# Kernel optimization log

Measured on AMD Instinct MI355X. Metric: run time of the kernel, lower is better.

## Reference

```python
import jax, jax.numpy as jnp
import numpy as np
from jax.scipy.special import logsumexp

EPS = 0.1
MAX_ITER = 50
THRESH = 1e-9


def _cost_matrix(x, y, p=2):
    # |x_i - y_j|^p summed over feature dim -> (N, P1, P2)
    return jnp.sum(jnp.abs(x[:, :, None, :] - y[:, None, :, :]) ** p, axis=-1)


def _sinkhorn_uv(C, eps, max_iter):
    # Log-domain Sinkhorn iterations; C is treated as a constant (torch no_grad).
    N, P1, P2 = C.shape
    log_mu = jnp.log(jnp.full((N, P1), 1.0 / P1, C.dtype) + 1e-8)
    log_nu = jnp.log(jnp.full((N, P2), 1.0 / P2, C.dtype) + 1e-8)

    def M(u, v):
        return (-C + u[:, :, None] + v[:, None, :]) / eps

    def cond(state):
        u, v, err, it = state
        return jnp.logical_and(it < max_iter, err >= THRESH)

    def body(state):
        u, v, err, it = state
        u1 = u
        u = eps * (log_mu - logsumexp(M(u, v), axis=-1)) + u
        v = eps * (log_nu - logsumexp(M(u, v), axis=-2)) + v
        err = jnp.mean(jnp.sum(jnp.abs(u - u1), axis=-1))
        return (u, v, err, it + 1)

    u0 = jnp.zeros((N, P1), C.dtype)
    v0 = jnp.zeros((N, P2), C.dtype)
    u, v, _, _ = jax.lax.while_loop(cond, body, (u0, v0, jnp.inf, 0))
    return u, v


def setup_inputs() -> dict:
    key = jax.random.key(0)
    kx, ky = jax.random.split(key)
    x = jax.random.normal(kx, (4, 2048, 64), dtype=jnp.float32)
    y = jax.random.normal(ky, (4, 2048, 64), dtype=jnp.float32)
    return {"x": x, "y": y}


def reference(x, y):
    C = _cost_matrix(x, y)
    # u, v computed under no_grad in torch -> constants w.r.t. x, y
    U, V = _sinkhorn_uv(jax.lax.stop_gradient(C), EPS, MAX_ITER)
    pi = jnp.exp((-C + U[:, :, None] + V[:, None, :]) / EPS)
    cost = jnp.sum(pi * C, axis=(-2, -1))  # reduction='none' -> (N,)
    return (cost, pi, C)
```

## Files before the change

### kernel.cpp

```cpp
#include <hip/hip_runtime.h>
#include <math.h>

#define NB 4
#define P 2048
#define DF 64
#define EPS 0.1f
#define INV_EPS 10.0f
#define MAX_ITER 50
#define NBLK 256
#define TPB 512
#define TR 128
#define TC 256
#define SCALE 14.426950408889634f
#define C2N 0.069314718055994531f
#define RPF (NB * P * 8)
#define CPF (NB * P * 16)

typedef float vfloat4 __attribute__((ext_vector_type(4)));

#if __has_builtin(__builtin_amdgcn_exp2f)
#define EXP2(x) __builtin_amdgcn_exp2f(x)
#else
#define EXP2(x) exp2f(x)
#endif
#if __has_builtin(__builtin_amdgcn_logf)
#define LOG2(x) __builtin_amdgcn_logf(x)
#else
#define LOG2(x) log2f(x)
#endif

struct BuildMem { float xs[32 * 132]; float ys[32 * 260]; };
union IterBuf {
  float rin[8 * 132];
  float Ld[64 * 260];
  float cin[16 * 260];
};
struct SMem {
  union { BuildMem b; IterBuf ib; } u;
  float red[132];
  float vlds[2][260];
};

__device__ __forceinline__ void flag_store(unsigned* f, unsigned v) {
  __hip_atomic_store(f, v, __ATOMIC_RELAXED, __HIP_MEMORY_SCOPE_AGENT);
}
__device__ __forceinline__ unsigned flag_load(unsigned* f) {
  return __hip_atomic_load(f, __ATOMIC_RELAXED, __HIP_MEMORY_SCOPE_AGENT);
}
__device__ __forceinline__ void store_f2_agent(float* p, float a, float b) {
  unsigned long long bits =
      ((unsigned long long)__float_as_uint(b) << 32) | __float_as_uint(a);
  __hip_atomic_store((unsigned long long*)p, bits, __ATOMIC_RELAXED,
                     __HIP_MEMORY_SCOPE_AGENT);
}
__device__ __forceinline__ float2 load_f2_agent(const float* p) {
  unsigned long long bits = __hip_atomic_load((unsigned long long*)p,
      __ATOMIC_RELAXED, __HIP_MEMORY_SCOPE_AGENT);
  return make_float2(__uint_as_float((unsigned)bits),
                     __uint_as_float((unsigned)(bits >> 32)));
}
__device__ __forceinline__ void store_f_agent(float* p, float v) {
  __hip_atomic_store(p, v, __ATOMIC_RELAXED, __HIP_MEMORY_SCOPE_AGENT);
}

__device__ __forceinline__ void u_stage(
    int k, int t, int c8, int r0, int ti, int tj, int n,
    const float (&cr)[2][32], const float* vl,
    float* rpp, unsigned* rf_mine) {
  float vv[32];
#pragma unroll
  for (int i = 0; i < 32; ++i) vv[i] = vl[32 * (i >> 2) + 4 * c8 + (i & 3)];
  float Lr[2];
#pragma unroll
  for (int r = 0; r < 2; ++r) {
    float m = -3.4e38f;
#pragma unroll
    for (int i = 0; i < 32; ++i) m = fmaxf(m, vv[i] - cr[r][i]);
    m = fmaxf(m, __shfl_xor(m, 1));
    m = fmaxf(m, __shfl_xor(m, 2));
    m = fmaxf(m, __shfl_xor(m, 4));
    float s = 0.f;
#pragma unroll
    for (int i = 0; i < 32; ++i) s += EXP2(vv[i] - cr[r][i] - m);
    s += __shfl_xor(s, 1);
    s += __shfl_xor(s, 2);
    s += __shfl_xor(s, 4);
    Lr[r] = m + LOG2(s);
  }
  if (c8 == 0)
    store_f2_agent(rpp + ((n * 16 + ti) * 8 + tj) * TR + r0, Lr[0], Lr[1]);
  __threadfence_block();
  __syncthreads();
  if (t == 0) flag_store(rf_mine, (unsigned)(k + 1));
}

__device__ __forceinline__ void row_merge(
    int k, int t, int r0, int ti, int n,
    float (&Ucr)[2], const float* rpp, unsigned* rfb, SMem& sm, float l2mu) {
  if (t < 8) {
    while (flag_load(rfb + t) < (unsigned)(k + 1)) __builtin_amdgcn_s_sleep(1);
  }
  __syncthreads();
  {
    const int idx = 2 * t;
    float2 a = load_f2_agent(rpp + (n * 16 + ti) * 1024 + idx);
    const int j = idx >> 7, row = idx & 127;
    *(float2*)&sm.u.ib.rin[j * 132 + row] = a;
  }
  __syncthreads();
  if (t < 128) {
    float m = sm.u.ib.rin[t];
#pragma unroll
    for (int j = 1; j < 8; ++j) m = fmaxf(m, sm.u.ib.rin[j * 132 + t]);
    float s = 0.f;
#pragma unroll
    for (int j = 0; j < 8; ++j) s += EXP2(sm.u.ib.rin[j * 132 + t] - m);
    sm.red[t] = l2mu - (m + LOG2(s));
  }
  __syncthreads();
  Ucr[0] = sm.red[r0];
  Ucr[1] = sm.red[r0 + 1];
}

__device__ __forceinline__ void v_stage(
    int k, int t, int w, int gg, int c8, int ti, int tj, int n,
    const float (&cr)[2][32], const float (&Ucr)[2],
    float* cpp, unsigned* cf_mine, SMem& sm) {
  const int grp = 8 * w + gg;
#pragma unroll
  for (int i = 0; i < 32; ++i) {
    float a0 = Ucr[0] - cr[0][i];
    float a1 = Ucr[1] - cr[1][i];
    float pm = fmaxf(a0, a1);
    float ps = 1.f + EXP2(-fabsf(a0 - a1));
    sm.u.ib.Ld[grp * 260 + 32 * (i >> 2) + 4 * c8 + (i & 3)] = pm + LOG2(ps);
  }
  __syncthreads();
  if (t < TC) {
    float m = sm.u.ib.Ld[t];
#pragma unroll
    for (int g2 = 1; g2 < 64; ++g2) m = fmaxf(m, sm.u.ib.Ld[g2 * 260 + t]);
    float s = 0.f;
#pragma unroll
    for (int g2 = 0; g2 < 64; ++g2) s += EXP2(sm.u.ib.Ld[g2 * 260 + t] - m);
    store_f_agent(cpp + ((n * 8 + tj) * 16 + ti) * TC + t, m + LOG2(s));
  }
  __threadfence_block();
  __syncthreads();
  if (t == 0) flag_store(cf_mine, (unsigned)(k + 1));
}

__device__ __forceinline__ void col_merge(
    int k, int t, int tj, int n, float* vl,
    const float* cpp, unsigned* cfb, SMem& sm, float l2mu) {
  if (t < 16) {
    while (flag_load(cfb + t) < (unsigned)(k + 1)) __builtin_amdgcn_s_sleep(1);
  }
  __syncthreads();
  {
    const int idx = 8 * t;
    const int jj = idx >> 8, col = idx & 255;
    const float* src = cpp + (n * 8 + tj) * 4096 + idx;
    float2 a = load_f2_agent(src);
    float2 b2 = load_f2_agent(src + 2);
    float2 c2 = load_f2_agent(src + 4);
    float2 d2 = load_f2_agent(src + 6);
    vfloat4 v0 = {a.x, a.y, b2.x, b2.y};
    vfloat4 v1 = {c2.x, c2.y, d2.x, d2.y};
    *(vfloat4*)&sm.u.ib.cin[jj * 260 + col] = v0;
    *(vfloat4*)&sm.u.ib.cin[jj * 260 + col + 4] = v1;
  }
  __syncthreads();
  if (t < TC) {
    float m = sm.u.ib.cin[t];
#pragma unroll
    for (int j = 1; j < 16; ++j) m = fmaxf(m, sm.u.ib.cin[j * 260 + t]);
    float s = 0.f;
#pragma unroll
    for (int j = 0; j < 16; ++j) s += EXP2(sm.u.ib.cin[j * 260 + t] - m);
    vl[t] = l2mu - (m + LOG2(s));
  }
  __syncthreads();
}

__global__ __launch_bounds__(TPB, 2) void sinkhorn_all(
    const float* __restrict__ x, const float* __restrict__ y,
    float* __restrict__ Cout, float* __restrict__ pi,
    float* __restrict__ cost, float* __restrict__ rp,
    float* __restrict__ cp, unsigned* __restrict__ flags, float l2mu) {
  __shared__ SMem sm;
  const int t = threadIdx.x;
  const int w = t >> 6;
  const int l = t & 63;
  const int gg = l >> 3;
  const int c8 = l & 7;
  const int b = blockIdx.x;
  const int g = b >> 7;
  const int idx = b & 127;
  const int ti = idx >> 3;
  const int tj = idx & 7;
  const int nA = 2 * g, nB = 2 * g + 1;
  const int r0 = 16 * w + 2 * gg;
  unsigned* rfA_mine = flags + (nA * 16 + ti) * 8 + tj;
  unsigned* rfB_mine = flags + (nB * 16 + ti) * 8 + tj;
  unsigned* rfA_band = flags + (nA * 16 + ti) * 8;
  unsigned* rfB_band = flags + (nB * 16 + ti) * 8;
  unsigned* cfA_mine = flags + 512 + (nA * 8 + tj) * 16 + ti;
  unsigned* cfB_mine = flags + 512 + (nB * 8 + tj) * 16 + ti;
  unsigned* cfA_band = flags + 512 + (nA * 8 + tj) * 16;
  unsigned* cfB_band = flags + 512 + (nB * 8 + tj) * 16;
  unsigned* ef = flags + 1024;

  float creg[2][2][32];
  float U[2][2];

#pragma unroll
  for (int c = 0; c < 2; ++c) {
    const int n = 2 * g + c;
    const size_t xyb = (size_t)n * P * DF;
#pragma unroll
    for (int r = 0; r < 2; ++r)
#pragma unroll
      for (int i = 0; i < 32; ++i) creg[c][r][i] = 0.f;
#pragma unroll
    for (int h = 0; h < 2; ++h) {
      __syncthreads();
      {
        const int cl = t >> 2, db = (t & 3) * 8;
        const float* xp = x + xyb + (size_t)(TR * ti + cl) * DF + 32 * h + db;
        float4 q0 = *(const float4*)(xp);
        float4 q1 = *(const float4*)(xp + 4);
        float* xs = sm.u.b.xs;
        xs[(db + 0) * 132 + cl] = q0.x; xs[(db + 1) * 132 + cl] = q0.y;
        xs[(db + 2) * 132 + cl] = q0.z; xs[(db + 3) * 132 + cl] = q0.w;
        xs[(db + 4) * 132 + cl] = q1.x; xs[(db + 5) * 132 + cl] = q1.y;
        xs[(db + 6) * 132 + cl] = q1.z; xs[(db + 7) * 132 + cl] = q1.w;
      }
      {
        const int cl = t >> 1, db = (t & 1) * 16;
        const float* yp = y + xyb + (size_t)(TC * tj + cl) * DF + 32 * h + db;
        float4 q0 = *(const float4*)(yp + 0);
        float4 q1 = *(const float4*)(yp + 4);
        float4 q2 = *(const float4*)(yp + 8);
        float4 q3 = *(const float4*)(yp + 12);
        float* ys = sm.u.b.ys;
        ys[(db + 0) * 260 + cl] = q0.x;  ys[(db + 1) * 260 + cl] = q0.y;
        ys[(db + 2) * 260 + cl] = q0.z;  ys[(db + 3) * 260 + cl] = q0.w;
        ys[(db + 4) * 260 + cl] = q1.x;  ys[(db + 5) * 260 + cl] = q1.y;
        ys[(db + 6) * 260 + cl] = q1.z;  ys[(db + 7) * 260 + cl] = q1.w;
        ys[(db + 8) * 260 + cl] = q2.x;  ys[(db + 9) * 260 + cl] = q2.y;
        ys[(db + 10) * 260 + cl] = q2.z; ys[(db + 11) * 260 + cl] = q2.w;
        ys[(db + 12) * 260 + cl] = q3.x; ys[(db + 13) * 260 + cl] = q3.y;
        ys[(db + 14) * 260 + cl] = q3.z; ys[(db + 15) * 260 + cl] = q3.w;
      }
      __syncthreads();
#pragma unroll 4
      for (int dd = 0; dd < 32; ++dd) {
        float2 x2 = *(const float2*)&sm.u.b.xs[dd * 132 + r0];
#pragma unroll
        for (int cc = 0; cc < 8; ++cc) {
          float4 y4 = *(const float4*)&sm.u.b.ys[dd * 260 + 32 * cc + 4 * c8];
          float d0, d1;
          d0 = x2.x - y4.x; creg[c][0][4*cc+0] = fmaf(d0, d0, creg[c][0][4*cc+0]);
          d1 = x2.y - y4.x; creg[c][1][4*cc+0] = fmaf(d1, d1, creg[c][1][4*cc+0]);
          d0 = x2.x - y4.y; creg[c][0][4*cc+1] = fmaf(d0, d0, creg[c][0][4*cc+1]);
          d1 = x2.y - y4.y; creg[c][1][4*cc+1] = fmaf(d1, d1, creg[c][1][4*cc+1]);
          d0 = x2.x - y4.z; creg[c][0][4*cc+2] = fmaf(d0, d0, creg[c][0][4*cc+2]);
          d1 = x2.y - y4.z; creg[c][1][4*cc+2] = fmaf(d1, d1, creg[c][1][4*cc+2]);
          d0 = x2.x - y4.w; creg[c][0][4*cc+3] = fmaf(d0, d0, creg[c][0][4*cc+3]);
          d1 = x2.y - y4.w; creg[c][1][4*cc+3] = fmaf(d1, d1, creg[c][1][4*cc+3]);
        }
      }
    }
    const size_t cb = (size_t)n * P * P;
#pragma unroll
    for (int r = 0; r < 2; ++r) {
      const size_t rowb = cb + (size_t)(TR * ti + r0 + r) * P + TC * tj;
#pragma unroll
      for (int cc = 0; cc < 8; ++cc) {
        vfloat4 c4 = {creg[c][r][4*cc+0], creg[c][r][4*cc+1],
                      creg[c][r][4*cc+2], creg[c][r][4*cc+3]};
        __builtin_nontemporal_store(c4, (vfloat4*)(Cout + rowb + 32*cc + 4*c8));
        creg[c][r][4*cc+0] *= SCALE;
        creg[c][r][4*cc+1] *= SCALE;
        creg[c][r][4*cc+2] *= SCALE;
        creg[c][r][4*cc+3] *= SCALE;
      }
    }
  }
  __syncthreads();
  if (t < 256) { sm.vlds[0][t] = 0.f; sm.vlds[1][t] = 0.f; }
  __syncthreads();

  float* vlA = sm.vlds[0];
  float* vlB = sm.vlds[1];
  u_stage(0, t, c8, r0, ti, tj, nA, creg[0], vlA, rp + RPF, rfA_mine);
  u_stage(0, t, c8, r0, ti, tj, nB, creg[1], vlB, rp + RPF, rfB_mine);
#pragma unroll 1
  for (int k = 0; k < MAX_ITER; ++k) {
    const int pw = (k + 1) & 1;
    float* rpp = rp + pw * RPF;
    float* cpp = cp + pw * CPF;
    float* rpn = rp + (k & 1) * RPF;
    row_merge(k, t, r0, ti, nA, U[0], rpp, rfA_band, sm, l2mu);
    v_stage(k, t, w, gg, c8, ti, tj, nA, creg[0], U[0], cpp, cfA_mine, sm);
    row_merge(k, t, r0, ti, nB, U[1], rpp, rfB_band, sm, l2mu);
    v_stage(k, t, w, gg, c8, ti, tj, nB, creg[1], U[1], cpp, cfB_mine, sm);
    col_merge(k, t, tj, nA, vlA, cpp, cfA_band, sm, l2mu);
    if (k + 1 < MAX_ITER)
      u_stage(k + 1, t, c8, r0, ti, tj, nA, creg[0], vlA, rpn, rfA_mine);
    col_merge(k, t, tj, nB, vlB, cpp, cfB_band, sm, l2mu);
    if (k + 1 < MAX_ITER)
      u_stage(k + 1, t, c8, r0, ti, tj, nB, creg[1], vlB, rpn, rfB_mine);
  }

  if (t == 0) flag_store(&ef[b], 1u);
  if (t < 256) {
    while (flag_load(&ef[t]) < 1u) __builtin_amdgcn_s_sleep(1);
  }
  __syncthreads();
#pragma unroll
  for (int c = 0; c < 2; ++c) {
    const int n = 2 * g + c;
    float vv[32];
#pragma unroll
    for (int i = 0; i < 32; ++i)
      vv[i] = sm.vlds[c][32 * (i >> 2) + 4 * c8 + (i & 3)];
    float csum = 0.f;
#pragma unroll
    for (int r = 0; r < 2; ++r) {
      const size_t rowb = (size_t)n * P * P + (size_t)(TR*ti + r0 + r) * P + TC*tj;
#pragma unroll
      for (int cc = 0; cc < 8; ++cc) {
        vfloat4 p4;
        p4.x = EXP2(U[c][r] + vv[4*cc+0] - creg[c][r][4*cc+0]);
        p4.y = EXP2(U[c][r] + vv[4*cc+1] - creg[c][r][4*cc+1]);
        p4.z = EXP2(U[c][r] + vv[4*cc+2] - creg[c][r][4*cc+2]);
        p4.w = EXP2(U[c][r] + vv[4*cc+3] - creg[c][r][4*cc+3]);
        csum += p4.x * creg[c][r][4*cc+0] + p4.y * creg[c][r][4*cc+1]
              + p4.z * creg[c][r][4*cc+2] + p4.w * creg[c][r][4*cc+3];
        __builtin_nontemporal_store(p4, (vfloat4*)(pi + rowb + 32*cc + 4*c8));
      }
    }
    float cs = csum * C2N;
#pragma unroll
    for (int off = 32; off; off >>= 1) cs += __shfl_xor(cs, off);
    if (l == 0) atomicAdd(cost + n, cs);
  }
}

__global__ __launch_bounds__(256) void build_c(const float* __restrict__ x,
                                               const float* __restrict__ y,
                                               float* __restrict__ C,
                                               float* __restrict__ CT) {
  __shared__ float xs[DF][68];
  __shared__ float ys[DF][68];
  const int n = blockIdx.z;
  const int i0 = blockIdx.y * 64, j0 = blockIdx.x * 64;
  const int t = threadIdx.x;
  const int lr = t >> 4, c4 = (t & 15) * 4;
  const size_t xb = (size_t)n * P * DF;
  for (int rr = lr; rr < 64; rr += 16) {
    float4 xv = *(const float4*)(x + xb + (size_t)(i0 + rr) * DF + c4);
    float4 yv = *(const float4*)(y + xb + (size_t)(j0 + rr) * DF + c4);
    xs[c4 + 0][rr] = xv.x; xs[c4 + 1][rr] = xv.y;
    xs[c4 + 2][rr] = xv.z; xs[c4 + 3][rr] = xv.w;
    ys[c4 + 0][rr] = yv.x; ys[c4 + 1][rr] = yv.y;
    ys[c4 + 2][rr] = yv.z; ys[c4 + 3][rr] = yv.w;
  }
  __syncthreads();
  const int ty = t >> 4, tx = t & 15;
  float acc[4][4];
#pragma unroll
  for (int e = 0; e < 4; ++e)
#pragma unroll
    for (int f = 0; f < 4; ++f) acc[e][f] = 0.f;
#pragma unroll 4
  for (int d = 0; d < DF; ++d) {
    float4 a4 = *(const float4*)&xs[d][4 * ty];
    float4 b4 = *(const float4*)&ys[d][4 * tx];
    float av[4] = {a4.x, a4.y, a4.z, a4.w};
    float bv[4] = {b4.x, b4.y, b4.z, b4.w};
#pragma unroll
    for (int e = 0; e < 4; ++e)
#pragma unroll
      for (int f = 0; f < 4; ++f) {
        float df = av[e] - bv[f];
        acc[e][f] = fmaf(df, df, acc[e][f]);
      }
  }
  const size_t cbase = (size_t)n * P * P;
#pragma unroll
  for (int e = 0; e < 4; ++e) {
    float4 v4 = make_float4(acc[e][0], acc[e][1], acc[e][2], acc[e][3]);
    *(float4*)(C + cbase + (size_t)(i0 + 4 * ty + e) * P + (j0 + 4 * tx)) = v4;
  }
#pragma unroll
  for (int f = 0; f < 4; ++f) {
    float4 v4 = make_float4(acc[0][f], acc[1][f], acc[2][f], acc[3][f]);
    *(float4*)(CT + cbase + (size_t)(j0 + 4 * tx + f) * P + (i0 + 4 * ty)) = v4;
  }
}

__global__ __launch_bounds__(256) void lse_pass(const float* __restrict__ M,
                                                const float* __restrict__ wv_,
                                                float* __restrict__ out,
                                                float log_w) {
  __shared__ float red[8];
  const int b = blockIdx.x;
  const int n = b >> 11;
  const int t = threadIdx.x;
  const float4* row = (const float4*)(M + (size_t)b * P);
  const float4* wv = (const float4*)(wv_ + (size_t)n * P);
  float4 c0 = row[t], c1 = row[t + 256];
  float4 w0 = wv[t], w1 = wv[t + 256];
  float a[8];
  a[0] = (w0.x - c0.x) * INV_EPS; a[1] = (w0.y - c0.y) * INV_EPS;
  a[2] = (w0.z - c0.z) * INV_EPS; a[3] = (w0.w - c0.w) * INV_EPS;
  a[4] = (w1.x - c1.x) * INV_EPS; a[5] = (w1.y - c1.y) * INV_EPS;
  a[6] = (w1.z - c1.z) * INV_EPS; a[7] = (w1.w - c1.w) * INV_EPS;
  float mx = a[0];
#pragma unroll
  for (int k = 1; k < 8; ++k) mx = fmaxf(mx, a[k]);
#pragma unroll
  for (int o = 32; o > 0; o >>= 1) mx = fmaxf(mx, __shfl_xor(mx, o));
  if ((t & 63) == 0) red[t >> 6] = mx;
  __syncthreads();
  mx = fmaxf(fmaxf(red[0], red[1]), fmaxf(red[2], red[3]));
  float s = 0.f;
#pragma unroll
  for (int k = 0; k < 8; ++k) s += __expf(a[k] - mx);
#pragma unroll
  for (int o = 32; o > 0; o >>= 1) s += __shfl_xor(s, o);
  if ((t & 63) == 0) red[4 + (t >> 6)] = s;
  __syncthreads();
  if (t == 0) {
    float S = red[4] + red[5] + red[6] + red[7];
    out[b] = EPS * (log_w - (mx + __logf(S)));
  }
}

__global__ __launch_bounds__(256) void final_pass(const float* __restrict__ C,
                                                  const float* __restrict__ u,
                                                  const float* __restrict__ v,
                                                  float* __restrict__ pi,
                                                  float* __restrict__ cost) {
  __shared__ float red[4];
  const int b = blockIdx.x;
  const int n = b >> 11;
  const int t = threadIdx.x;
  const float ui = u[b];
  const float4* row = (const float4*)(C + (size_t)b * P);
  const float4* vv = (const float4*)(v + (size_t)n * P);
  float4* prow = (float4*)(pi + (size_t)b * P);
  float local = 0.f;
#pragma unroll
  for (int h = 0; h < 2; ++h) {
    float4 c = row[t + 256 * h];
    float4 vw = vv[t + 256 * h];
    float4 p;
    p.x = __expf((ui + vw.x - c.x) * INV_EPS);
    p.y = __expf((ui + vw.y - c.y) * INV_EPS);
    p.z = __expf((ui + vw.z - c.z) * INV_EPS);
    p.w = __expf((ui + vw.w - c.w) * INV_EPS);
    prow[t + 256 * h] = p;
    local += p.x * c.x + p.y * c.y + p.z * c.z + p.w * c.w;
  }
#pragma unroll
  for (int o = 32; o > 0; o >>= 1) local += __shfl_xor(local, o);
  if ((t & 63) == 0) red[t >> 6] = local;
  __syncthreads();
  if (t == 0) {
    float S = red[0] + red[1] + red[2] + red[3];
    atomicAdd(cost + n, S);
  }
}

extern "C" void kernel_launch(void* const* d_in, const int* in_sizes, int n_in,
                              void* d_out, int out_size, void* d_ws, size_t ws_size,
                              hipStream_t stream) {
  const float* x = (const float*)d_in[0];
  const float* y = (const float*)d_in[1];
  float* cost = (float*)d_out;
  float* pi = cost + 4;
  float* C = pi + (size_t)NB * P * P;
  float* rp = pi;
  float* cp = pi + 2 * RPF;
  unsigned* flags = (unsigned*)d_ws;

  (void)hipMemsetAsync(cost, 0, NB * sizeof(float), stream);
  (void)hipMemsetAsync(flags, 0, 5120, stream);

  float lmu = logf(1.0f / (float)P + 1e-8f);
  float l2mu = log2f(1.0f / (float)P + 1e-8f);

  void* args[] = {(void*)&x, (void*)&y, (void*)&C, (void*)&pi,
                  (void*)&cost, (void*)&rp, (void*)&cp, (void*)&flags,
                  (void*)&l2mu};
  hipError_t err = hipLaunchCooperativeKernel((void*)sinkhorn_all, dim3(NBLK),
                                              dim3(TPB), args, 0, stream);
  if (err != hipSuccess) {
    float* u = (float*)d_ws;
    float* v = u + NB * P;
    (void)hipMemsetAsync(v, 0, NB * P * sizeof(float), stream);
    float* CT = pi;
    build_c<<<dim3(32, 32, 4), 256, 0, stream>>>(x, y, C, CT);
    for (int it = 0; it < MAX_ITER; ++it) {
      lse_pass<<<NB * P, 256, 0, stream>>>(C, v, u, lmu);
      lse_pass<<<NB * P, 256, 0, stream>>>(CT, u, v, lmu);
    }
    final_pass<<<NB * P, 256, 0, stream>>>(C, u, v, pi, cost);
  }
}
```

Before: 856.1 us.

## Halve column tile to double block count and parallelize LSE merges

Shrinks each block's column tile from 256 to 128 columns and launches 512 cooperative blocks instead of 256, with launch bounds raised to four blocks per CU. Partial-LSE buffers, flag layouts and band sizes are reorganized to match. The row, column and v-stage reductions now split each reduction across four threads and combine them with shuffle-based online-LSE merges, so more of the block does the work. This spreads the iterative Sinkhorn work over more CUs, at the cost of more inter-block flag traffic per iteration and a larger grid barrier that assumes all 512 blocks can be resident at once.

```diff
diff --git a/kernel.cpp b/kernel.cpp
--- a/kernel.cpp
+++ b/kernel.cpp
@@ -7,14 +7,14 @@
 #define EPS 0.1f
 #define INV_EPS 10.0f
 #define MAX_ITER 50
-#define NBLK 256
+#define NBLK 512
 #define TPB 512
 #define TR 128
-#define TC 256
+#define TC 128
 #define SCALE 14.426950408889634f
 #define C2N 0.069314718055994531f
-#define RPF (NB * P * 8)
-#define CPF (NB * P * 16)
+#define RPF (NB * 16 * 16 * 128)
+#define CPF (NB * 16 * 16 * 128)
 
 typedef float vfloat4 __attribute__((ext_vector_type(4)));
 
@@ -29,16 +29,16 @@
 #define LOG2(x) log2f(x)
 #endif
 
-struct BuildMem { float xs[32 * 132]; float ys[32 * 260]; };
+struct BuildMem { float xs[32 * 132]; float ys[32 * 132]; };
 union IterBuf {
-  float rin[8 * 132];
-  float Ld[64 * 260];
-  float cin[16 * 260];
+  float rin[16 * 132];
+  float Ld[64 * 133];
+  float cin[16 * 132];
 };
 struct SMem {
   union { BuildMem b; IterBuf ib; } u;
   float red[132];
-  float vlds[2][260];
+  float vlds[2][132];
 };
 
 __device__ __forceinline__ void flag_store(unsigned* f, unsigned v) {
@@ -63,32 +63,43 @@
   __hip_atomic_store(p, v, __ATOMIC_RELAXED, __HIP_MEMORY_SCOPE_AGENT);
 }
 
+__device__ __forceinline__ void lse_merge(float& M, float& S, float om, float os) {
+  float d = EXP2(-fabsf(M - om));
+  float Sn = (M >= om) ? fmaf(os, d, S) : fmaf(S, d, os);
+  M = fmaxf(M, om);
+  S = Sn;
+}
+
 __device__ __forceinline__ void u_stage(
     int k, int t, int c8, int r0, int ti, int tj, int n,
-    const float (&cr)[2][32], const float* vl,
+    const float (&cr)[2][16], const float* vl,
     float* rpp, unsigned* rf_mine) {
-  float vv[32];
-#pragma unroll
-  for (int i = 0; i < 32; ++i) vv[i] = vl[32 * (i >> 2) + 4 * c8 + (i & 3)];
+  float vv[16];
+#pragma unroll
+  for (int i = 0; i < 16; ++i) vv[i] = vl[32 * (i >> 2) + 4 * c8 + (i & 3)];
   float Lr[2];
 #pragma unroll
   for (int r = 0; r < 2; ++r) {
+    float d[16];
     float m = -3.4e38f;
 #pragma unroll
-    for (int i = 0; i < 32; ++i) m = fmaxf(m, vv[i] - cr[r][i]);
+    for (int i = 0; i < 16; ++i) {
+      d[i] = vv[i] - cr[r][i];
+      m = fmaxf(m, d[i]);
+    }
     m = fmaxf(m, __shfl_xor(m, 1));
     m = fmaxf(m, __shfl_xor(m, 2));
     m = fmaxf(m, __shfl_xor(m, 4));
     float s = 0.f;
 #pragma unroll
-    for (int i = 0; i < 32; ++i) s += EXP2(vv[i] - cr[r][i] - m);
+    for (int i = 0; i < 16; ++i) s += EXP2(d[i] - m);
     s += __shfl_xor(s, 1);
     s += __shfl_xor(s, 2);
     s += __shfl_xor(s, 4);
     Lr[r] = m + LOG2(s);
   }
   if (c8 == 0)
-    store_f2_agent(rpp + ((n * 16 + ti) * 8 + tj) * TR + r0, Lr[0], Lr[1]);
+    store_f2_agent(rpp + ((n * 16 + ti) * 16 + tj) * TR + r0, Lr[0], Lr[1]);
   __threadfence_block();
   __syncthreads();
   if (t == 0) flag_store(rf_mine, (unsigned)(k + 1));
@@ -97,25 +108,33 @@
 __device__ __forceinline__ void row_merge(
     int k, int t, int r0, int ti, int n,
     float (&Ucr)[2], const float* rpp, unsigned* rfb, SMem& sm, float l2mu) {
-  if (t < 8) {
+  if (t < 16) {
     while (flag_load(rfb + t) < (unsigned)(k + 1)) __builtin_amdgcn_s_sleep(1);
   }
   __syncthreads();
   {
-    const int idx = 2 * t;
-    float2 a = load_f2_agent(rpp + (n * 16 + ti) * 1024 + idx);
-    const int j = idx >> 7, row = idx & 127;
+    const int idx = 4 * t;
+    const int j = t >> 5, row = idx & 127;
+    const float* src = rpp + (n * 16 + ti) * 2048 + idx;
+    float2 a = load_f2_agent(src);
+    float2 b2 = load_f2_agent(src + 2);
     *(float2*)&sm.u.ib.rin[j * 132 + row] = a;
-  }
-  __syncthreads();
-  if (t < 128) {
-    float m = sm.u.ib.rin[t];
-#pragma unroll
-    for (int j = 1; j < 8; ++j) m = fmaxf(m, sm.u.ib.rin[j * 132 + t]);
-    float s = 0.f;
-#pragma unroll
-    for (int j = 0; j < 8; ++j) s += EXP2(sm.u.ib.rin[j * 132 + t] - m);
-    sm.red[t] = l2mu - (m + LOG2(s));
+    *(float2*)&sm.u.ib.rin[j * 132 + row + 2] = b2;
+  }
+  __syncthreads();
+  {
+    const int row = t >> 2, q = t & 3;
+    float L0 = sm.u.ib.rin[(4 * q + 0) * 132 + row];
+    float L1 = sm.u.ib.rin[(4 * q + 1) * 132 + row];
+    float L2 = sm.u.ib.rin[(4 * q + 2) * 132 + row];
+    float L3 = sm.u.ib.rin[(4 * q + 3) * 132 + row];
+    float M = fmaxf(fmaxf(L0, L1), fmaxf(L2, L3));
+    float S = EXP2(L0 - M) + EXP2(L1 - M) + EXP2(L2 - M) + EXP2(L3 - M);
+    float Mo = __shfl_xor(M, 1), So = __shfl_xor(S, 1);
+    lse_merge(M, S, Mo, So);
+    Mo = __shfl_xor(M, 2); So = __shfl_xor(S, 2);
+    lse_merge(M, S, Mo, So);
+    if (q == 0) sm.red[row] = l2mu - (M + LOG2(S));
   }
   __syncthreads();
   Ucr[0] = sm.red[r0];
@@ -124,27 +143,38 @@
 
 __device__ __forceinline__ void v_stage(
     int k, int t, int w, int gg, int c8, int ti, int tj, int n,
-    const float (&cr)[2][32], const float (&Ucr)[2],
+    const float (&cr)[2][16], const float (&Ucr)[2],
     float* cpp, unsigned* cf_mine, SMem& sm) {
   const int grp = 8 * w + gg;
 #pragma unroll
-  for (int i = 0; i < 32; ++i) {
+  for (int i = 0; i < 16; ++i) {
     float a0 = Ucr[0] - cr[0][i];
     float a1 = Ucr[1] - cr[1][i];
     float pm = fmaxf(a0, a1);
     float ps = 1.f + EXP2(-fabsf(a0 - a1));
-    sm.u.ib.Ld[grp * 260 + 32 * (i >> 2) + 4 * c8 + (i & 3)] = pm + LOG2(ps);
-  }
-  __syncthreads();
-  if (t < TC) {
-    float m = sm.u.ib.Ld[t];
-#pragma unroll
-    for (int g2 = 1; g2 < 64; ++g2) m = fmaxf(m, sm.u.ib.Ld[g2 * 260 + t]);
-    float s = 0.f;
-#pragma unroll
-    for (int g2 = 0; g2 < 64; ++g2) s += EXP2(sm.u.ib.Ld[g2 * 260 + t] - m);
-    store_f_agent(cpp + ((n * 8 + tj) * 16 + ti) * TC + t, m + LOG2(s));
-  }
+    sm.u.ib.Ld[grp * 133 + 32 * (i >> 2) + 4 * c8 + (i & 3)] = pm + LOG2(ps);
+  }
+  __syncthreads();
+  {
+    const int col = t >> 2, q = t & 3;
+    float L[16];
+#pragma unroll
+    for (int z = 0; z < 16; ++z) L[z] = sm.u.ib.Ld[(16 * q + z) * 133 + col];
+    float M = L[0];
+#pragma unroll
+    for (int z = 1; z < 16; ++z) M = fmaxf(M, L[z]);
+    float S = 0.f;
+#pragma unroll
+    for (int z = 0; z < 16; ++z) S += EXP2(L[z] - M);
+    float Mo = __shfl_xor(M, 1), So = __shfl_xor(S, 1);
+    lse_merge(M, S, Mo, So);
+    Mo = __shfl_xor(M, 2); So = __shfl_xor(S, 2);
+    lse_merge(M, S, Mo, So);
+    if (q == 0) sm.red[col] = M + LOG2(S);
+  }
+  __syncthreads();
+  if (t < TC)
+    store_f_agent(cpp + ((n * 16 + tj) * 16 + ti) * TC + t, sm.red[t]);
   __threadfence_block();
   __syncthreads();
   if (t == 0) flag_store(cf_mine, (unsigned)(k + 1));
@@ -158,32 +188,33 @@
   }
   __syncthreads();
   {
-    const int idx = 8 * t;
-    const int jj = idx >> 8, col = idx & 255;
-    const float* src = cpp + (n * 8 + tj) * 4096 + idx;
+    const int idx = 4 * t;
+    const int j = t >> 5, col = idx & 127;
+    const float* src = cpp + (n * 16 + tj) * 2048 + idx;
     float2 a = load_f2_agent(src);
     float2 b2 = load_f2_agent(src + 2);
-    float2 c2 = load_f2_agent(src + 4);
-    float2 d2 = load_f2_agent(src + 6);
-    vfloat4 v0 = {a.x, a.y, b2.x, b2.y};
-    vfloat4 v1 = {c2.x, c2.y, d2.x, d2.y};
-    *(vfloat4*)&sm.u.ib.cin[jj * 260 + col] = v0;
-    *(vfloat4*)&sm.u.ib.cin[jj * 260 + col + 4] = v1;
-  }
-  __syncthreads();
-  if (t < TC) {
-    float m = sm.u.ib.cin[t];
-#pragma unroll
-    for (int j = 1; j < 16; ++j) m = fmaxf(m, sm.u.ib.cin[j * 260 + t]);
-    float s = 0.f;
-#pragma unroll
-    for (int j = 0; j < 16; ++j) s += EXP2(sm.u.ib.cin[j * 260 + t] - m);
-    vl[t] = l2mu - (m + LOG2(s));
-  }
-  __syncthreads();
-}
-
-__global__ __launch_bounds__(TPB, 2) void sinkhorn_all(
+    *(float2*)&sm.u.ib.cin[j * 132 + col] = a;
+    *(float2*)&sm.u.ib.cin[j * 132 + col + 2] = b2;
+  }
+  __syncthreads();
+  {
+    const int col = t >> 2, q = t & 3;
+    float L0 = sm.u.ib.cin[(4 * q + 0) * 132 + col];
+    float L1 = sm.u.ib.cin[(4 * q + 1) * 132 + col];
+    float L2 = sm.u.ib.cin[(4 * q + 2) * 132 + col];
+    float L3 = sm.u.ib.cin[(4 * q + 3) * 132 + col];
+    float M = fmaxf(fmaxf(L0, L1), fmaxf(L2, L3));
+    float S = EXP2(L0 - M) + EXP2(L1 - M) + EXP2(L2 - M) + EXP2(L3 - M);
+    float Mo = __shfl_xor(M, 1), So = __shfl_xor(S, 1);
+    lse_merge(M, S, Mo, So);
+    Mo = __shfl_xor(M, 2); So = __shfl_xor(S, 2);
+    lse_merge(M, S, Mo, So);
+    if (q == 0) vl[col] = l2mu - (M + LOG2(S));
+  }
+  __syncthreads();
+}
+
+__global__ __launch_bounds__(TPB, 4) void sinkhorn_all(
     const float* __restrict__ x, const float* __restrict__ y,
     float* __restrict__ Cout, float* __restrict__ pi,
     float* __restrict__ cost, float* __restrict__ rp,
@@ -195,23 +226,23 @@
   const int gg = l >> 3;
   const int c8 = l & 7;
   const int b = blockIdx.x;
-  const int g = b >> 7;
-  const int idx = b & 127;
-  const int ti = idx >> 3;
-  const int tj = idx & 7;
+  const int g = b >> 8;
+  const int idx = b & 255;
+  const int ti = idx >> 4;
+  const int tj = idx & 15;
   const int nA = 2 * g, nB = 2 * g + 1;
   const int r0 = 16 * w + 2 * gg;
-  unsigned* rfA_mine = flags + (nA * 16 + ti) * 8 + tj;
-  unsigned* rfB_mine = flags + (nB * 16 + ti) * 8 + tj;
-  unsigned* rfA_band = flags + (nA * 16 + ti) * 8;
-  unsigned* rfB_band = flags + (nB * 16 + ti) * 8;
-  unsigned* cfA_mine = flags + 512 + (nA * 8 + tj) * 16 + ti;
-  unsigned* cfB_mine = flags + 512 + (nB * 8 + tj) * 16 + ti;
-  unsigned* cfA_band = flags + 512 + (nA * 8 + tj) * 16;
-  unsigned* cfB_band = flags + 512 + (nB * 8 + tj) * 16;
-  unsigned* ef = flags + 1024;
-
-  float creg[2][2][32];
+  unsigned* rfA_mine = flags + (nA * 16 + ti) * 16 + tj;
+  unsigned* rfB_mine = flags + (nB * 16 + ti) * 16 + tj;
+  unsigned* rfA_band = flags + (nA * 16 + ti) * 16;
+  unsigned* rfB_band = flags + (nB * 16 + ti) * 16;
+  unsigned* cfA_mine = flags + 1024 + (nA * 16 + tj) * 16 + ti;
+  unsigned* cfB_mine = flags + 1024 + (nB * 16 + tj) * 16 + ti;
+  unsigned* cfA_band = flags + 1024 + (nA * 16 + tj) * 16;
+  unsigned* cfB_band = flags + 1024 + (nB * 16 + tj) * 16;
+  unsigned* ef = flags + 2048;
+
+  float creg[2][2][16];
   float U[2][2];
 
 #pragma unroll
@@ -221,7 +252,7 @@
 #pragma unroll
     for (int r = 0; r < 2; ++r)
 #pragma unroll
-      for (int i = 0; i < 32; ++i) creg[c][r][i] = 0.f;
+      for (int i = 0; i < 16; ++i) creg[c][r][i] = 0.f;
 #pragma unroll
     for (int h = 0; h < 2; ++h) {
       __syncthreads();
@@ -235,31 +266,22 @@
         xs[(db + 2) * 132 + cl] = q0.z; xs[(db + 3) * 132 + cl] = q0.w;
         xs[(db + 4) * 132 + cl] = q1.x; xs[(db + 5) * 132 + cl] = q1.y;
         xs[(db + 6) * 132 + cl] = q1.z; xs[(db + 7) * 132 + cl] = q1.w;
-      }
-      {
-        const int cl = t >> 1, db = (t & 1) * 16;
         const float* yp = y + xyb + (size_t)(TC * tj + cl) * DF + 32 * h + db;
-        float4 q0 = *(const float4*)(yp + 0);
-        float4 q1 = *(const float4*)(yp + 4);
-        float4 q2 = *(const float4*)(yp + 8);
-        float4 q3 = *(const float4*)(yp + 12);
+        q0 = *(const float4*)(yp);
+        q1 = *(const float4*)(yp + 4);
         float* ys = sm.u.b.ys;
-        ys[(db + 0) * 260 + cl] = q0.x;  ys[(db + 1) * 260 + cl] = q0.y;
-        ys[(db + 2) * 260 + cl] = q0.z;  ys[(db + 3) * 260 + cl] = q0.w;
-        ys[(db + 4) * 260 + cl] = q1.x;  ys[(db + 5) * 260 + cl] = q1.y;
-        ys[(db + 6) * 260 + cl] = q1.z;  ys[(db + 7) * 260 + cl] = q1.w;
-        ys[(db + 8) * 260 + cl] = q2.x;  ys[(db + 9) * 260 + cl] = q2.y;
-        ys[(db + 10) * 260 + cl] = q2.z; ys[(db + 11) * 260 + cl] = q2.w;
-        ys[(db + 12) * 260 + cl] = q3.x; ys[(db + 13) * 260 + cl] = q3.y;
-        ys[(db + 14) * 260 + cl] = q3.z; ys[(db + 15) * 260 + cl] = q3.w;
+        ys[(db + 0) * 132 + cl] = q0.x; ys[(db + 1) * 132 + cl] = q0.y;
+        ys[(db + 2) * 132 + cl] = q0.z; ys[(db + 3) * 132 + cl] = q0.w;
+        ys[(db + 4) * 132 + cl] = q1.x; ys[(db + 5) * 132 + cl] = q1.y;
+        ys[(db + 6) * 132 + cl] = q1.z; ys[(db + 7) * 132 + cl] = q1.w;
       }
       __syncthreads();
 #pragma unroll 4
       for (int dd = 0; dd < 32; ++dd) {
         float2 x2 = *(const float2*)&sm.u.b.xs[dd * 132 + r0];
 #pragma unroll
-        for (int cc = 0; cc < 8; ++cc) {
-          float4 y4 = *(const float4*)&sm.u.b.ys[dd * 260 + 32 * cc + 4 * c8];
+        for (int cc = 0; cc < 4; ++cc) {
+          float4 y4 = *(const float4*)&sm.u.b.ys[dd * 132 + 32 * cc + 4 * c8];
           float d0, d1;
           d0 = x2.x - y4.x; creg[c][0][4*cc+0] = fmaf(d0, d0, creg[c][0][4*cc+0]);
           d1 = x2.y - y4.x; creg[c][1][4*cc+0] = fmaf(d1, d1, creg[c][1][4*cc+0]);
@@ -277,7 +299,7 @@
     for (int r = 0; r < 2; ++r) {
       const size_t rowb = cb + (size_t)(TR * ti + r0 + r) * P + TC * tj;
 #pragma unroll
-      for (int cc = 0; cc < 8; ++cc) {
+      for (int cc = 0; cc < 4; ++cc) {
         vfloat4 c4 = {creg[c][r][4*cc+0], creg[c][r][4*cc+1],
                       creg[c][r][4*cc+2], creg[c][r][4*cc+3]};
         __builtin_nontemporal_store(c4, (vfloat4*)(Cout + rowb + 32*cc + 4*c8));
@@ -289,7 +311,7 @@
     }
   }
   __syncthreads();
-  if (t < 256) { sm.vlds[0][t] = 0.f; sm.vlds[1][t] = 0.f; }
+  if (t < 132) { sm.vlds[0][t] = 0.f; sm.vlds[1][t] = 0.f; }
   __syncthreads();
 
   float* vlA = sm.vlds[0];
@@ -315,23 +337,23 @@
   }
 
   if (t == 0) flag_store(&ef[b], 1u);
-  if (t < 256) {
+  {
     while (flag_load(&ef[t]) < 1u) __builtin_amdgcn_s_sleep(1);
   }
   __syncthreads();
 #pragma unroll
   for (int c = 0; c < 2; ++c) {
     const int n = 2 * g + c;
-    float vv[32];
-#pragma unroll
-    for (int i = 0; i < 32; ++i)
+    float vv[16];
+#pragma unroll
+    for (int i = 0; i < 16; ++i)
       vv[i] = sm.vlds[c][32 * (i >> 2) + 4 * c8 + (i & 3)];
     float csum = 0.f;
 #pragma unroll
     for (int r = 0; r < 2; ++r) {
       const size_t rowb = (size_t)n * P * P + (size_t)(TR*ti + r0 + r) * P + TC*tj;
 #pragma unroll
-      for (int cc = 0; cc < 8; ++cc) {
+      for (int cc = 0; cc < 4; ++cc) {
         vfloat4 p4;
         p4.x = EXP2(U[c][r] + vv[4*cc+0] - creg[c][r][4*cc+0]);
         p4.y = EXP2(U[c][r] + vv[4*cc+1] - creg[c][r][4*cc+1]);
@@ -489,7 +511,7 @@
   unsigned* flags = (unsigned*)d_ws;
 
   (void)hipMemsetAsync(cost, 0, NB * sizeof(float), stream);
-  (void)hipMemsetAsync(flags, 0, 5120, stream);
+  (void)hipMemsetAsync(flags, 0, 10240, stream);
 
   float lmu = logf(1.0f / (float)P + 1e-8f);
   float l2mu = log2f(1.0f / (float)P + 1e-8f);
```

After: 911.4 us. 1.06x slower.
